# Kernel tuning notes

Measured on AMD Instinct MI355X. Metric: run time of the kernel, lower is better.

The kernel has to match this reference:

```python
import jax, jax.numpy as jnp
import numpy as np

BATCH, D_INNER, DT_RANK, N = 256, 5120, 160, 16

def _softplus_thresh(z, threshold=20.0):
    # softplus(z) with beta=1; linear above threshold (matches ttnn.softplus(parameter1=1, parameter2=20))
    return jnp.where(z > threshold, z, jax.nn.softplus(z))

def setup_inputs() -> dict:
    key = jax.random.key(0)
    ks = jax.random.split(key, 9)
    s = lambda d: 1.0 / np.sqrt(d)
    return {
        "x": jax.random.normal(ks[0], (1, 1, BATCH, D_INNER), jnp.float32),
        "h": jax.random.normal(ks[1], (BATCH, D_INNER, N), jnp.float32) * 0.1,
        "W_delta": jax.random.normal(ks[2], (D_INNER, DT_RANK), jnp.float32) * s(D_INNER),
        "W_dt": jax.random.normal(ks[3], (DT_RANK, D_INNER), jnp.float32) * s(DT_RANK),
        "b_dt": jax.random.normal(ks[4], (D_INNER,), jnp.float32) * 0.1,
        "A_log": jax.random.uniform(ks[5], (D_INNER, N), jnp.float32, 0.0, 1.5),
        "W_B": jax.random.normal(ks[6], (D_INNER, N), jnp.float32) * s(D_INNER),
        "W_C": jax.random.normal(ks[7], (D_INNER, N), jnp.float32) * s(D_INNER),
        "D": jax.random.normal(ks[8], (D_INNER,), jnp.float32),
    }

def reference(x, h, W_delta, W_dt, b_dt, A_log, W_B, W_C, D):
    # x: (1,1,B,d_inner) single decode step; h: (B,d_inner,n) SSM state
    xb = x.reshape(BATCH, D_INNER)                           # (B, d)
    # delta = softplus(x @ W_delta @ W_dt + b_dt)           -> (B, d)
    dt = _softplus_thresh((xb @ W_delta) @ W_dt + b_dt)
    A = -jnp.exp(A_log)                                      # (d, n)
    abar = jnp.exp(dt[:, :, None] * A[None, :, :])           # (B, d, n)
    Bp = xb @ W_B                                            # (B, n)
    # bbar * x: delta * B * x, broadcast over state dim
    bx = (dt * xb)[:, :, None] * Bp[:, None, :]              # (B, d, n)
    h_new = abar * h + bx                                    # (B, d, n) new hidden state
    C = xb @ W_C                                             # (B, n)
    y = jnp.einsum("bdn,bn->bd", h_new, C) + xb * D          # readout + skip (D)
    return y.reshape(1, 1, BATCH, D_INNER)
```

## Files before the change

kernel.cpp:

```cpp
#include <hip/hip_runtime.h>
#include <math.h>

#define BATCH 256
#define DIN   5120
#define RANK  160
#define NS    16
#define NCAT  192
#define NSPLIT 40

__global__ __launch_bounds__(256) void k1a_gemm(
    const float* __restrict__ x, const float* __restrict__ Wd,
    const float* __restrict__ WB, const float* __restrict__ WC,
    float* __restrict__ psum)
{
    __shared__ float xT[32][64];
    __shared__ float Wt[32][64];
    const int t  = threadIdx.x;
    const int m0 = blockIdx.x * 64;
    const int n0 = blockIdx.y * 64;
    const int z  = blockIdx.z;
    const int k0 = z * 128;
    const int tm = (t >> 4) * 4;
    const int tn = (t & 15) * 4;

    const int lm  = t >> 2;
    const int lk  = (t & 3) * 8;
    const int ln  = t & 63;
    const int lkb = (t >> 6) * 8;

    const float* wsrc; int wstr;
    {
        const int c = n0 + ln;
        if (c < RANK)            { wsrc = Wd + c;                wstr = RANK; }
        else if (c < RANK + NS)  { wsrc = WB + (c - RANK);       wstr = NS;   }
        else                     { wsrc = WC + (c - RANK - NS);  wstr = NS;   }
    }

    float acc[4][4] = {{0.f}};

    for (int ks = 0; ks < 4; ++ks) {
        const int kb = k0 + ks * 32;
        {
            const float* src = x + (size_t)(m0 + lm) * DIN + kb + lk;
            const float4 a0 = *(const float4*)src;
            const float4 a1 = *(const float4*)(src + 4);
            xT[lk+0][lm]=a0.x; xT[lk+1][lm]=a0.y; xT[lk+2][lm]=a0.z; xT[lk+3][lm]=a0.w;
            xT[lk+4][lm]=a1.x; xT[lk+5][lm]=a1.y; xT[lk+6][lm]=a1.z; xT[lk+7][lm]=a1.w;
        }
        {
            const float* wp = wsrc + (size_t)(kb + lkb) * wstr;
            #pragma unroll
            for (int i = 0; i < 8; ++i) { Wt[lkb + i][ln] = *wp; wp += wstr; }
        }
        __syncthreads();
        #pragma unroll
        for (int k = 0; k < 32; ++k) {
            const float4 a = *(const float4*)&xT[k][tm];
            const float4 b = *(const float4*)&Wt[k][tn];
            acc[0][0] += a.x*b.x; acc[0][1] += a.x*b.y; acc[0][2] += a.x*b.z; acc[0][3] += a.x*b.w;
            acc[1][0] += a.y*b.x; acc[1][1] += a.y*b.y; acc[1][2] += a.y*b.z; acc[1][3] += a.y*b.w;
            acc[2][0] += a.z*b.x; acc[2][1] += a.z*b.y; acc[2][2] += a.z*b.z; acc[2][3] += a.z*b.w;
            acc[3][0] += a.w*b.x; acc[3][1] += a.w*b.y; acc[3][2] += a.w*b.z; acc[3][3] += a.w*b.w;
        }
        __syncthreads();
    }

    float* dst = psum + (size_t)z * (BATCH * NCAT);
    #pragma unroll
    for (int i = 0; i < 4; ++i) {
        const int gm = m0 + tm + i;
        float4 o; o.x = acc[i][0]; o.y = acc[i][1]; o.z = acc[i][2]; o.w = acc[i][3];
        *(float4*)&dst[(size_t)gm * NCAT + n0 + tn] = o;
    }
}

__global__ __launch_bounds__(256) void k1r_reduce(
    const float* __restrict__ psum, const float* __restrict__ A_log,
    float* __restrict__ P, float* __restrict__ Bp, float* __restrict__ Cc,
    float* __restrict__ A2t)
{
    const int g = blockIdx.x * 256 + threadIdx.x;
    A2t[g] = -1.442695041f * __expf(A_log[g]);

    if (blockIdx.x < NCAT) {
        const int o = blockIdx.x * 256 + threadIdx.x;
        float s = 0.f;
        #pragma unroll 8
        for (int z = 0; z < NSPLIT; ++z) s += psum[(size_t)z * (BATCH * NCAT) + o];
        const int gm = o / NCAT;
        const int gc = o - gm * NCAT;
        if (gc < RANK)           P [gm * RANK + gc]             = s;
        else if (gc < RANK + NS) Bp[gm * NS   + gc - RANK]      = s;
        else                     Cc[gm * NS   + gc - RANK - NS] = s;
    }
}

__device__ __forceinline__ float softplus20(float z)
{
    if (z > 20.f) return z;
    return fmaxf(z, 0.f) + log1pf(__expf(-fabsf(z)));
}

__global__ __launch_bounds__(256) void k2_dt(
    const float* __restrict__ P, const float* __restrict__ Wdt,
    const float* __restrict__ bdt, float* __restrict__ dtw)
{
    __shared__ float aT[32][64];
    __shared__ float Bt[32][64];

    const int t  = threadIdx.x;
    const int c0 = blockIdx.x * 64;
    const int b0 = blockIdx.y * 64;

    const int tm = (t >> 4) * 4;
    const int tn = (t & 15) * 4;
    const int lm  = t >> 2;
    const int lk  = (t & 3) * 8;
    const int ln  = t & 63;
    const int lkb = (t >> 6) * 8;

    float acc[4][4] = {{0.f}};

    for (int ks = 0; ks < 5; ++ks) {
        const int kb = ks * 32;
        {
            const float* src = P + (size_t)(b0 + lm) * RANK + kb + lk;
            const float4 a0 = *(const float4*)src;
            const float4 a1 = *(const float4*)(src + 4);
            aT[lk+0][lm]=a0.x; aT[lk+1][lm]=a0.y; aT[lk+2][lm]=a0.z; aT[lk+3][lm]=a0.w;
            aT[lk+4][lm]=a1.x; aT[lk+5][lm]=a1.y; aT[lk+6][lm]=a1.z; aT[lk+7][lm]=a1.w;
        }
        {
            const float* wp = Wdt + (size_t)(kb + lkb) * DIN + c0 + ln;
            #pragma unroll
            for (int i = 0; i < 8; ++i) { Bt[lkb + i][ln] = wp[(size_t)i * DIN]; }
        }
        __syncthreads();
        #pragma unroll
        for (int k = 0; k < 32; ++k) {
            const float4 a = *(const float4*)&aT[k][tm];
            const float4 b = *(const float4*)&Bt[k][tn];
            acc[0][0] += a.x*b.x; acc[0][1] += a.x*b.y; acc[0][2] += a.x*b.z; acc[0][3] += a.x*b.w;
            acc[1][0] += a.y*b.x; acc[1][1] += a.y*b.y; acc[1][2] += a.y*b.z; acc[1][3] += a.y*b.w;
            acc[2][0] += a.z*b.x; acc[2][1] += a.z*b.y; acc[2][2] += a.z*b.z; acc[2][3] += a.z*b.w;
            acc[3][0] += a.w*b.x; acc[3][1] += a.w*b.y; acc[3][2] += a.w*b.z; acc[3][3] += a.w*b.w;
        }
        __syncthreads();
    }

    const float4 bz = *(const float4*)&bdt[c0 + tn];
    #pragma unroll
    for (int i = 0; i < 4; ++i) {
        float4 o;
        o.x = softplus20(acc[i][0] + bz.x);
        o.y = softplus20(acc[i][1] + bz.y);
        o.z = softplus20(acc[i][2] + bz.z);
        o.w = softplus20(acc[i][3] + bz.w);
        *(float4*)&dtw[(size_t)(b0 + tm + i) * DIN + c0 + tn] = o;
    }
}

__global__ __launch_bounds__(256) void k3_ssm(
    const float* __restrict__ dtw, const float* __restrict__ x,
    const float* __restrict__ h, const float* __restrict__ A2t,
    const float* __restrict__ Bp, const float* __restrict__ Cc,
    const float* __restrict__ Dv, float* __restrict__ y)
{
    const int t    = threadIdx.x;
    const int lane = t & 63;
    const int wv   = t >> 6;
    const int c0   = blockIdx.x * 64;
    const int b0   = (blockIdx.y * 4 + wv) * 4;
    const int v    = lane & 3;
    const int j    = lane >> 2;

    float4 A2q[4]; float dvq[4];
    #pragma unroll
    for (int q = 0; q < 4; ++q) {
        const int c = c0 + q * 16 + j;
        A2q[q] = *(const float4*)(A2t + (size_t)c * NS + v * 4);
        dvq[q] = Dv[c];
    }

    #pragma unroll
    for (int bi = 0; bi < 4; ++bi) {
        const int gb = b0 + bi;
        const float4 B4 = *(const float4*)(Bp + gb * NS + v * 4);
        const float4 C4 = *(const float4*)(Cc + gb * NS + v * 4);
        float res[4];
        #pragma unroll
        for (int q = 0; q < 4; ++q) {
            const int c = c0 + q * 16 + j;
            const float dtv = dtw[(size_t)gb * DIN + c];
            const float xv  = x[(size_t)gb * DIN + c];
            const float dtx = dtv * xv;
            const float4 h4 = *(const float4*)(h + ((size_t)gb * DIN + c) * NS + v * 4);
            float s;
            s  = (exp2f(dtv * A2q[q].x) * h4.x + dtx * B4.x) * C4.x;
            s += (exp2f(dtv * A2q[q].y) * h4.y + dtx * B4.y) * C4.y;
            s += (exp2f(dtv * A2q[q].z) * h4.z + dtx * B4.z) * C4.z;
            s += (exp2f(dtv * A2q[q].w) * h4.w + dtx * B4.w) * C4.w;
            if (v == 0) s += xv * dvq[q];
            res[q] = s;
        }
        #pragma unroll
        for (int q = 0; q < 4; ++q) {
            res[q] += __shfl_xor(res[q], 1, 64);
            res[q] += __shfl_xor(res[q], 2, 64);
        }
        const float out = (v == 0) ? res[0] : (v == 1) ? res[1]
                        : (v == 2) ? res[2] : res[3];
        y[(size_t)gb * DIN + c0 + v * 16 + j] = out;
    }
}

extern "C" void kernel_launch(void* const* d_in, const int* in_sizes, int n_in,
                              void* d_out, int out_size, void* d_ws, size_t ws_size,
                              hipStream_t stream)
{
    const float* x     = (const float*)d_in[0];
    const float* h     = (const float*)d_in[1];
    const float* Wd    = (const float*)d_in[2];
    const float* Wdt   = (const float*)d_in[3];
    const float* bdt   = (const float*)d_in[4];
    const float* A_log = (const float*)d_in[5];
    const float* WB    = (const float*)d_in[6];
    const float* WC    = (const float*)d_in[7];
    const float* Dv    = (const float*)d_in[8];
    float* out = (float*)d_out;

    float* psum = (float*)d_ws;
    float* dtw  = psum;
    float* P    = psum + (size_t)NSPLIT * BATCH * NCAT;
    float* Bp   = P  + BATCH * RANK;
    float* Cc   = Bp + BATCH * NS;
    float* A2t  = Cc + BATCH * NS;

    k1a_gemm  <<<dim3(4, 3, NSPLIT), 256, 0, stream>>>(x, Wd, WB, WC, psum);
    k1r_reduce<<<dim3(320),          256, 0, stream>>>(psum, A_log, P, Bp, Cc, A2t);
    k2_dt     <<<dim3(80, 4),        256, 0, stream>>>(P, Wdt, bdt, dtw);
    k3_ssm    <<<dim3(80, 16),       256, 0, stream>>>(dtw, x, h, A2t, Bp, Cc, Dv, out);
}
```

Baseline: 182.3 us.

## Stage h through LDS with double-buffered async loads in SSM kernel

Rewrites the SSM readout kernel so each lane owns one channel and loops over all 16 state entries. The h tile is staged into shared memory with double-buffered global_load_lds copies, so the next batch group is fetched while the current one is computed. The B·C dot product is factored out algebraically, which removes the cross-lane shuffle reduction. In exchange the kernel uses 32KB of LDS per block, adds a block barrier per stage, and each lane now does 16 exp2f per batch row with redundant B/C loads.

```diff
diff --git a/kernel.cpp b/kernel.cpp
--- a/kernel.cpp
+++ b/kernel.cpp
@@ -166,52 +166,86 @@
     const float* __restrict__ Bp, const float* __restrict__ Cc,
     const float* __restrict__ Dv, float* __restrict__ y)
 {
+    __shared__ float hbuf[2][4096];
+
     const int t    = threadIdx.x;
     const int lane = t & 63;
     const int wv   = t >> 6;
     const int c0   = blockIdx.x * 64;
-    const int b0   = (blockIdx.y * 4 + wv) * 4;
-    const int v    = lane & 3;
-    const int j    = lane >> 2;
-
-    float4 A2q[4]; float dvq[4];
+    const int b0   = blockIdx.y * 16;
+    const int c    = c0 + lane;
+
+    const float4* a2p = (const float4*)(A2t + (size_t)c * NS);
+    const float4 A20 = a2p[0], A21 = a2p[1], A22 = a2p[2], A23 = a2p[3];
+    const float  Dval = Dv[c];
+
+    #define STAGE(T) do {                                                       \
+        const float* srcr = h + ((size_t)(b0 + (T)*4 + wv) * DIN + c0) * NS;    \
+        float* ldsb = &hbuf[(T)&1][wv * 1024];                                  \
+        __builtin_amdgcn_global_load_lds(                                       \
+            (const __attribute__((address_space(1))) void*)(srcr + 0*256 + lane*4), \
+            (__attribute__((address_space(3))) void*)(ldsb + 0*256), 16, 0, 0); \
+        __builtin_amdgcn_global_load_lds(                                       \
+            (const __attribute__((address_space(1))) void*)(srcr + 1*256 + lane*4), \
+            (__attribute__((address_space(3))) void*)(ldsb + 1*256), 16, 0, 0); \
+        __builtin_amdgcn_global_load_lds(                                       \
+            (const __attribute__((address_space(1))) void*)(srcr + 2*256 + lane*4), \
+            (__attribute__((address_space(3))) void*)(ldsb + 2*256), 16, 0, 0); \
+        __builtin_amdgcn_global_load_lds(                                       \
+            (const __attribute__((address_space(1))) void*)(srcr + 3*256 + lane*4), \
+            (__attribute__((address_space(3))) void*)(ldsb + 3*256), 16, 0, 0); \
+    } while (0)
+
+    STAGE(0);
+    __syncthreads();
+
     #pragma unroll
-    for (int q = 0; q < 4; ++q) {
-        const int c = c0 + q * 16 + j;
-        A2q[q] = *(const float4*)(A2t + (size_t)c * NS + v * 4);
-        dvq[q] = Dv[c];
-    }
-
-    #pragma unroll
-    for (int bi = 0; bi < 4; ++bi) {
-        const int gb = b0 + bi;
-        const float4 B4 = *(const float4*)(Bp + gb * NS + v * 4);
-        const float4 C4 = *(const float4*)(Cc + gb * NS + v * 4);
-        float res[4];
+    for (int T = 0; T < 4; ++T) {
+        if (T < 3) STAGE(T + 1);
+
         #pragma unroll
-        for (int q = 0; q < 4; ++q) {
-            const int c = c0 + q * 16 + j;
-            const float dtv = dtw[(size_t)gb * DIN + c];
-            const float xv  = x[(size_t)gb * DIN + c];
-            const float dtx = dtv * xv;
-            const float4 h4 = *(const float4*)(h + ((size_t)gb * DIN + c) * NS + v * 4);
-            float s;
-            s  = (exp2f(dtv * A2q[q].x) * h4.x + dtx * B4.x) * C4.x;
-            s += (exp2f(dtv * A2q[q].y) * h4.y + dtx * B4.y) * C4.y;
-            s += (exp2f(dtv * A2q[q].z) * h4.z + dtx * B4.z) * C4.z;
-            s += (exp2f(dtv * A2q[q].w) * h4.w + dtx * B4.w) * C4.w;
-            if (v == 0) s += xv * dvq[q];
-            res[q] = s;
-        }
-        #pragma unroll
-        for (int q = 0; q < 4; ++q) {
-            res[q] += __shfl_xor(res[q], 1, 64);
-            res[q] += __shfl_xor(res[q], 2, 64);
-        }
-        const float out = (v == 0) ? res[0] : (v == 1) ? res[1]
-                        : (v == 2) ? res[2] : res[3];
-        y[(size_t)gb * DIN + c0 + v * 16 + j] = out;
-    }
+        for (int u = 0; u < 4; ++u) {
+            const int b = b0 + T * 4 + u;
+            const size_t bc = (size_t)b * DIN + c;
+            const float dtv = dtw[bc];
+            const float xv  = x[bc];
+            const float4* bp4 = (const float4*)(Bp + b * NS);
+            const float4* cc4 = (const float4*)(Cc + b * NS);
+            const float4 Bq0 = bp4[0], Bq1 = bp4[1], Bq2 = bp4[2], Bq3 = bp4[3];
+            const float4 Cq0 = cc4[0], Cq1 = cc4[1], Cq2 = cc4[2], Cq3 = cc4[3];
+
+            const float4* hv = (const float4*)&hbuf[T & 1][u * 1024 + lane * 16];
+            const float4 h0 = hv[0], h1 = hv[1], h2 = hv[2], h3 = hv[3];
+
+            float sbc;
+            sbc  = Bq0.x*Cq0.x + Bq0.y*Cq0.y + Bq0.z*Cq0.z + Bq0.w*Cq0.w;
+            sbc += Bq1.x*Cq1.x + Bq1.y*Cq1.y + Bq1.z*Cq1.z + Bq1.w*Cq1.w;
+            sbc += Bq2.x*Cq2.x + Bq2.y*Cq2.y + Bq2.z*Cq2.z + Bq2.w*Cq2.w;
+            sbc += Bq3.x*Cq3.x + Bq3.y*Cq3.y + Bq3.z*Cq3.z + Bq3.w*Cq3.w;
+
+            float s = xv * (dtv * sbc + Dval);
+            s += exp2f(dtv * A20.x) * h0.x * Cq0.x;
+            s += exp2f(dtv * A20.y) * h0.y * Cq0.y;
+            s += exp2f(dtv * A20.z) * h0.z * Cq0.z;
+            s += exp2f(dtv * A20.w) * h0.w * Cq0.w;
+            s += exp2f(dtv * A21.x) * h1.x * Cq1.x;
+            s += exp2f(dtv * A21.y) * h1.y * Cq1.y;
+            s += exp2f(dtv * A21.z) * h1.z * Cq1.z;
+            s += exp2f(dtv * A21.w) * h1.w * Cq1.w;
+            s += exp2f(dtv * A22.x) * h2.x * Cq2.x;
+            s += exp2f(dtv * A22.y) * h2.y * Cq2.y;
+            s += exp2f(dtv * A22.z) * h2.z * Cq2.z;
+            s += exp2f(dtv * A22.w) * h2.w * Cq2.w;
+            s += exp2f(dtv * A23.x) * h3.x * Cq3.x;
+            s += exp2f(dtv * A23.y) * h3.y * Cq3.y;
+            s += exp2f(dtv * A23.z) * h3.z * Cq3.z;
+            s += exp2f(dtv * A23.w) * h3.w * Cq3.w;
+
+            y[bc] = s;
+        }
+        __syncthreads();
+    }
+    #undef STAGE
 }
 
 extern "C" void kernel_launch(void* const* d_in, const int* in_sizes, int n_in,
```

Result: slower. 193.6 us (+6.2%).

## Fuse dt GEMM and softplus into SSM kernel, compute A inline

Applied to the files above, without the earlier changes.

Removes the separate k2_dt kernel. Each SSM block now computes its 16x64 tile of dt from P and W_dt directly into shared memory, applies softplus, and uses it right away. The A = -exp(A_log) precompute also moves from the reduce kernel into the SSM kernel. This drops one launch and the dtw global round-trip. In exchange, each W_dt column tile is re-read by 16 batch-row blocks instead of 4, and the small GEMM uses a less register-blocked inner loop.

```diff
diff --git a/kernel.cpp b/kernel.cpp
--- a/kernel.cpp
+++ b/kernel.cpp
@@ -75,24 +75,18 @@
 }
 
 __global__ __launch_bounds__(256) void k1r_reduce(
-    const float* __restrict__ psum, const float* __restrict__ A_log,
-    float* __restrict__ P, float* __restrict__ Bp, float* __restrict__ Cc,
-    float* __restrict__ A2t)
-{
-    const int g = blockIdx.x * 256 + threadIdx.x;
-    A2t[g] = -1.442695041f * __expf(A_log[g]);
-
-    if (blockIdx.x < NCAT) {
-        const int o = blockIdx.x * 256 + threadIdx.x;
-        float s = 0.f;
-        #pragma unroll 8
-        for (int z = 0; z < NSPLIT; ++z) s += psum[(size_t)z * (BATCH * NCAT) + o];
-        const int gm = o / NCAT;
-        const int gc = o - gm * NCAT;
-        if (gc < RANK)           P [gm * RANK + gc]             = s;
-        else if (gc < RANK + NS) Bp[gm * NS   + gc - RANK]      = s;
-        else                     Cc[gm * NS   + gc - RANK - NS] = s;
-    }
+    const float* __restrict__ psum,
+    float* __restrict__ P, float* __restrict__ Bp, float* __restrict__ Cc)
+{
+    const int o = blockIdx.x * 256 + threadIdx.x;
+    float s = 0.f;
+    #pragma unroll 8
+    for (int z = 0; z < NSPLIT; ++z) s += psum[(size_t)z * (BATCH * NCAT) + o];
+    const int gm = o / NCAT;
+    const int gc = o - gm * NCAT;
+    if (gc < RANK)           P [gm * RANK + gc]             = s;
+    else if (gc < RANK + NS) Bp[gm * NS   + gc - RANK]      = s;
+    else                     Cc[gm * NS   + gc - RANK - NS] = s;
 }
 
 __device__ __forceinline__ float softplus20(float z)
@@ -101,97 +95,84 @@
     return fmaxf(z, 0.f) + log1pf(__expf(-fabsf(z)));
 }
 
-__global__ __launch_bounds__(256) void k2_dt(
+__global__ __launch_bounds__(256) void k3_ssm(
     const float* __restrict__ P, const float* __restrict__ Wdt,
-    const float* __restrict__ bdt, float* __restrict__ dtw)
-{
-    __shared__ float aT[32][64];
-    __shared__ float Bt[32][64];
-
-    const int t  = threadIdx.x;
-    const int c0 = blockIdx.x * 64;
-    const int b0 = blockIdx.y * 64;
-
-    const int tm = (t >> 4) * 4;
-    const int tn = (t & 15) * 4;
-    const int lm  = t >> 2;
-    const int lk  = (t & 3) * 8;
-    const int ln  = t & 63;
-    const int lkb = (t >> 6) * 8;
-
-    float acc[4][4] = {{0.f}};
-
-    for (int ks = 0; ks < 5; ++ks) {
-        const int kb = ks * 32;
-        {
-            const float* src = P + (size_t)(b0 + lm) * RANK + kb + lk;
-            const float4 a0 = *(const float4*)src;
-            const float4 a1 = *(const float4*)(src + 4);
-            aT[lk+0][lm]=a0.x; aT[lk+1][lm]=a0.y; aT[lk+2][lm]=a0.z; aT[lk+3][lm]=a0.w;
-            aT[lk+4][lm]=a1.x; aT[lk+5][lm]=a1.y; aT[lk+6][lm]=a1.z; aT[lk+7][lm]=a1.w;
-        }
-        {
-            const float* wp = Wdt + (size_t)(kb + lkb) * DIN + c0 + ln;
-            #pragma unroll
-            for (int i = 0; i < 8; ++i) { Bt[lkb + i][ln] = wp[(size_t)i * DIN]; }
-        }
-        __syncthreads();
-        #pragma unroll
-        for (int k = 0; k < 32; ++k) {
-            const float4 a = *(const float4*)&aT[k][tm];
-            const float4 b = *(const float4*)&Bt[k][tn];
-            acc[0][0] += a.x*b.x; acc[0][1] += a.x*b.y; acc[0][2] += a.x*b.z; acc[0][3] += a.x*b.w;
-            acc[1][0] += a.y*b.x; acc[1][1] += a.y*b.y; acc[1][2] += a.y*b.z; acc[1][3] += a.y*b.w;
-            acc[2][0] += a.z*b.x; acc[2][1] += a.z*b.y; acc[2][2] += a.z*b.z; acc[2][3] += a.z*b.w;
-            acc[3][0] += a.w*b.x; acc[3][1] += a.w*b.y; acc[3][2] += a.w*b.z; acc[3][3] += a.w*b.w;
-        }
-        __syncthreads();
-    }
-
-    const float4 bz = *(const float4*)&bdt[c0 + tn];
-    #pragma unroll
-    for (int i = 0; i < 4; ++i) {
-        float4 o;
-        o.x = softplus20(acc[i][0] + bz.x);
-        o.y = softplus20(acc[i][1] + bz.y);
-        o.z = softplus20(acc[i][2] + bz.z);
-        o.w = softplus20(acc[i][3] + bz.w);
-        *(float4*)&dtw[(size_t)(b0 + tm + i) * DIN + c0 + tn] = o;
-    }
-}
-
-__global__ __launch_bounds__(256) void k3_ssm(
-    const float* __restrict__ dtw, const float* __restrict__ x,
-    const float* __restrict__ h, const float* __restrict__ A2t,
+    const float* __restrict__ bdt, const float* __restrict__ x,
+    const float* __restrict__ h, const float* __restrict__ A_log,
     const float* __restrict__ Bp, const float* __restrict__ Cc,
     const float* __restrict__ Dv, float* __restrict__ y)
 {
+    __shared__ float sP[16 * RANK];
+    __shared__ float Bt[32][64];
+    __shared__ float sdt[16][64];
+
     const int t    = threadIdx.x;
     const int lane = t & 63;
     const int wv   = t >> 6;
     const int c0   = blockIdx.x * 64;
-    const int b0   = (blockIdx.y * 4 + wv) * 4;
-    const int v    = lane & 3;
-    const int j    = lane >> 2;
+    const int b0   = blockIdx.y * 16;
+
+    {
+        const float* Pb = P + (size_t)b0 * RANK;
+        #pragma unroll
+        for (int i = 0; i < 10; ++i) sP[i * 256 + t] = Pb[i * 256 + t];
+
+        const int ln  = lane;
+        const int lkb = wv * 8;
+        float acc[4] = {0.f, 0.f, 0.f, 0.f};
+
+        for (int ks = 0; ks < 5; ++ks) {
+            const int kb = ks * 32;
+            {
+                const float* wp = Wdt + (size_t)(kb + lkb) * DIN + c0 + ln;
+                #pragma unroll
+                for (int i = 0; i < 8; ++i) Bt[lkb + i][ln] = wp[(size_t)i * DIN];
+            }
+            __syncthreads();
+            #pragma unroll
+            for (int k = 0; k < 32; ++k) {
+                const float w = Bt[k][lane];
+                acc[0] += sP[(wv * 4 + 0) * RANK + kb + k] * w;
+                acc[1] += sP[(wv * 4 + 1) * RANK + kb + k] * w;
+                acc[2] += sP[(wv * 4 + 2) * RANK + kb + k] * w;
+                acc[3] += sP[(wv * 4 + 3) * RANK + kb + k] * w;
+            }
+            __syncthreads();
+        }
+
+        const float bz = bdt[c0 + lane];
+        #pragma unroll
+        for (int i = 0; i < 4; ++i)
+            sdt[wv * 4 + i][lane] = softplus20(acc[i] + bz);
+    }
+    __syncthreads();
+
+    const int v = lane & 3;
+    const int j = lane >> 2;
 
     float4 A2q[4]; float dvq[4];
     #pragma unroll
     for (int q = 0; q < 4; ++q) {
         const int c = c0 + q * 16 + j;
-        A2q[q] = *(const float4*)(A2t + (size_t)c * NS + v * 4);
+        const float4 al = *(const float4*)(A_log + (size_t)c * NS + v * 4);
+        A2q[q].x = -1.442695041f * __expf(al.x);
+        A2q[q].y = -1.442695041f * __expf(al.y);
+        A2q[q].z = -1.442695041f * __expf(al.z);
+        A2q[q].w = -1.442695041f * __expf(al.w);
         dvq[q] = Dv[c];
     }
 
     #pragma unroll
     for (int bi = 0; bi < 4; ++bi) {
-        const int gb = b0 + bi;
+        const int bl = wv * 4 + bi;
+        const int gb = b0 + bl;
         const float4 B4 = *(const float4*)(Bp + gb * NS + v * 4);
         const float4 C4 = *(const float4*)(Cc + gb * NS + v * 4);
         float res[4];
         #pragma unroll
         for (int q = 0; q < 4; ++q) {
             const int c = c0 + q * 16 + j;
-            const float dtv = dtw[(size_t)gb * DIN + c];
+            const float dtv = sdt[bl][q * 16 + j];
             const float xv  = x[(size_t)gb * DIN + c];
             const float dtx = dtv * xv;
             const float4 h4 = *(const float4*)(h + ((size_t)gb * DIN + c) * NS + v * 4);
@@ -230,14 +211,12 @@
     float* out = (float*)d_out;
 
     float* psum = (float*)d_ws;
-    float* dtw  = psum;
     float* P    = psum + (size_t)NSPLIT * BATCH * NCAT;
     float* Bp   = P  + BATCH * RANK;
     float* Cc   = Bp + BATCH * NS;
-    float* A2t  = Cc + BATCH * NS;
 
     k1a_gemm  <<<dim3(4, 3, NSPLIT), 256, 0, stream>>>(x, Wd, WB, WC, psum);
-    k1r_reduce<<<dim3(320),          256, 0, stream>>>(psum, A_log, P, Bp, Cc, A2t);
-    k2_dt     <<<dim3(80, 4),        256, 0, stream>>>(P, Wdt, bdt, dtw);
-    k3_ssm    <<<dim3(80, 16),       256, 0, stream>>>(dtw, x, h, A2t, Bp, Cc, Dv, out);
-}
+    k1r_reduce<<<dim3(NCAT),         256, 0, stream>>>(psum, P, Bp, Cc);
+    k3_ssm    <<<dim3(80, 16),       256, 0, stream>>>(P, Wdt, bdt, x, h, A_log,
+                                                       Bp, Cc, Dv, out);
+}
```

Result: faster. 174.5 us (-4.3%).
